# Optimization experiments

Hardware: AMD Instinct MI355X
Metric: run time of the kernel (lower is better)

## Reference

```python
import jax, jax.numpy as jnp
import numpy as np

B, SD, AD, M, MAXC = 65536, 32, 1, 32, 2  # batch, state_dim, action_dim, msg_dim, max_children


def _l2norm(x):
    # F.normalize(x, dim=-1) with eps=1e-12
    return x / jnp.maximum(jnp.linalg.norm(x, axis=-1, keepdims=True), 1e-12)


def _mlp(x, w1, b1, w2, b2, w3, b3):
    # MLPBase: Linear->ReLU->Linear->ReLU->Linear (400/300 hidden)
    h = jax.nn.relu(x @ w1 + b1)
    h = jax.nn.relu(h @ w2 + b2)
    return h @ w3 + b3


def setup_inputs() -> dict:
    key = jax.random.key(0)
    ks = iter(jax.random.split(key, 40))

    def p(shape):
        return jax.random.normal(next(ks), shape, jnp.float32) * 0.05

    inp = {
        "state": jax.random.normal(next(ks), (B, SD), jnp.float32),
        "action": jax.random.normal(next(ks), (B, AD), jnp.float32),
        # CriticUp params
        "up_fc1_w": p((SD + AD, 64)), "up_fc1_b": p((64,)),
        "up_fc2_w": p((64 + M, 64)), "up_fc2_b": p((64,)),
        "up_fc3_w": p((64, M)), "up_fc3_b": p((M,)),
        "att_w": p((9 + SD, M)), "att_b": p((M,)),
    }
    q_in = 12 + M + AD + M   # rel_pos(12) + self_input(msg_dim) + action + msg_down
    m_in = 12 + M + M        # rel_pos(12) + self_input + msg_down
    for n, d, out in (("q1", q_in, 1), ("q2", q_in, 1), ("msg", m_in, M * MAXC)):
        inp[n + "_w1"] = p((d, 400)); inp[n + "_b1"] = p((400,))
        inp[n + "_w2"] = p((400, 300)); inp[n + "_b2"] = p((300,))
        inp[n + "_w3"] = p((300, out)); inp[n + "_b3"] = p((out,))
    return inp


def reference(state, action,
              up_fc1_w, up_fc1_b, up_fc2_w, up_fc2_b, up_fc3_w, up_fc3_b,
              att_w, att_b,
              q1_w1, q1_b1, q1_w2, q1_b2, q1_w3, q1_b3,
              q2_w1, q2_b1, q2_w2, q2_b2, q2_w3, q2_b3,
              msg_w1, msg_b1, msg_w2, msg_b2, msg_w3, msg_b3):
    b = state.shape[0]
    # ---- bottom-up (num_limbs=1: root has no children -> zero child states/messages) ----
    xu = _l2norm(jnp.concatenate([state, action], -1) @ up_fc1_w + up_fc1_b)  # [b,64]
    ch_states = jnp.zeros((b, MAXC, 9 + SD), state.dtype)
    att = jax.nn.softmax(ch_states @ att_w + att_b, axis=-2)                  # [b,MAXC,M]
    m_up = (jnp.zeros((b, MAXC, M), state.dtype) * att).sum(-2)              # [b,M] (zeros)
    h = jnp.tanh(jnp.concatenate([xu, m_up], -1))
    h = jnp.tanh(h @ up_fc2_w + up_fc2_b)
    msg_up = _l2norm(h @ up_fc3_w + up_fc3_b)                                 # [b,M]
    # ---- top-down (root's parent index -1 wraps to itself -> zero relative offsets) ----
    pos = state[:, :3]
    rel = jnp.concatenate([jnp.zeros((b, 6), state.dtype), pos, pos], -1)     # [b,12]
    m_td = jnp.zeros((b, M), state.dtype)                                     # sliced from zero parent_msg
    xum = jnp.concatenate([rel, msg_up, action, m_td], -1)
    x1 = _mlp(xum, q1_w1, q1_b1, q1_w2, q1_b2, q1_w3, q1_b3)                  # [b,1]
    x2 = _mlp(xum, q2_w1, q2_b1, q2_w2, q2_b2, q2_w3, q2_b3)                  # [b,1]
    xm = jnp.tanh(jnp.concatenate([rel, msg_up, m_td], -1))
    msg_down = _l2norm(_mlp(xm, msg_w1, msg_b1, msg_w2, msg_b2, msg_w3, msg_b3))
    del msg_down  # computed per torch forward but unused in single-limb output
    # stack over 1 limb then sum over limb dim == identity
    return (x1, x2)
```

## Files before the change

### kernel.cpp

```cpp
#include <hip/hip_runtime.h>
#include <math.h>


#define BTOT   65536
#define XUM_OFF 655360ull

#define PK_BLK  78
#define PH_THR  512
#define PH_ROWS 128
#define PH_BLK  (BTOT / PH_ROWS)
#define F1W 0
#define F1B 2112
#define F2W 2176
#define F2B 6272
#define F3W 6336
#define F3B 8384
#define W0_FLOATS 8416

#define ML_THR  512
#define ML_ROWS 64
#define ML_BLK  (BTOT / ML_ROWS)
#define H1S     428

typedef float  f32x4 __attribute__((ext_vector_type(4)));
typedef __bf16 bf16x8 __attribute__((ext_vector_type(8)));
typedef unsigned short u16x8 __attribute__((ext_vector_type(8)));
typedef unsigned short u16x4 __attribute__((ext_vector_type(4)));
typedef unsigned int   u32x2 __attribute__((ext_vector_type(2)));

__device__ __forceinline__ unsigned short f2b(float f) {
  union { float f; unsigned int u; } v; v.f = f;
  return (unsigned short)((v.u + 0x7fffu + ((v.u >> 16) & 1u)) >> 16);
}
__device__ __forceinline__ float b2f(unsigned short u) {
  union { unsigned int u; float f; } v; v.u = ((unsigned int)u) << 16;
  return v.f;
}
__device__ __forceinline__ f32x4 MFMA(bf16x8 a, bf16x8 b, f32x4 c) {
  return __builtin_amdgcn_mfma_f32_16x16x32_bf16(a, b, c, 0, 0, 0);
}
__device__ __forceinline__ bf16x8 ld8(const unsigned short* p) {
  return __builtin_bit_cast(bf16x8, *(const u16x8*)p);
}
__device__ __forceinline__ float ftanh(float x) {
  float e = __builtin_amdgcn_exp2f(x * 2.885390081777927f);
  return (e - 1.0f) * __builtin_amdgcn_rcpf(e + 1.0f);
}

struct P0 {
  const float* state; const float* action;
  const float* f1w; const float* f1b;
  const float* f2w; const float* f2b;
  const float* f3w; const float* f3b;
  const float* q1w1; const float* q1b1; const float* q1w2;
  const float* q2w1; const float* q2b1; const float* q2w2;
  unsigned short* ws;
  unsigned short* xum;
};

__global__ __launch_bounds__(PH_THR, 4) void phase0_kernel(P0 P) {
  __shared__ float w0[W0_FLOATS];
  __shared__ unsigned short hx[PH_ROWS * 68];
  const int tid = threadIdx.x;

  if (blockIdx.x < PK_BLK) {
    const int gid = blockIdx.x * PH_THR + tid;
    const int lane = gid & 63, f = gid >> 6;
    const int q = f / 312, fl = f - q * 312;
    const float* w1 = q ? P.q2w1 : P.q1w1;
    const float* b1 = q ? P.q2b1 : P.q1b1;
    const float* w2 = q ? P.q2w2 : P.q1w2;
    int nt, ks; const bool isw1 = (fl < 52);
    if (isw1) { nt = fl >> 1; ks = fl & 1; }
    else      { int fl2 = fl - 52; nt = fl2 / 13; ks = fl2 - nt * 13; }
    const int col = nt * 16 + (lane & 15);
    const int k0  = ks * 32 + (lane >> 4) * 8;
    unsigned short v[8];
    #pragma unroll
    for (int j = 0; j < 8; ++j) {
      const int k = k0 + j;
      float x = 0.f;
      if (isw1) {
        if (col < 400) {
          if (k < 39) x = w1[(6 + k) * 400 + col];
          else if (k == 39) x = b1[col];
        }
      } else {
        if (k < 400 && col < 300) x = w2[k * 300 + col];
      }
      v[j] = f2b(x);
    }
    *(u16x8*)(P.ws + (size_t)f * 512 + lane * 8) = *(const u16x8*)v;
    return;
  }

  const int row = tid >> 2, sub = tid & 3, j0 = sub * 16;
  const long grow = (long)(blockIdx.x - PK_BLK) * PH_ROWS + row;

  for (int i = tid; i < 528;  i += PH_THR) *(f32x4*)(w0 + F1W + 4*i) = *(const f32x4*)(P.f1w + 4*i);
  for (int i = tid; i < 16;   i += PH_THR) *(f32x4*)(w0 + F1B + 4*i) = *(const f32x4*)(P.f1b + 4*i);
  for (int i = tid; i < 1024; i += PH_THR) *(f32x4*)(w0 + F2W + 4*i) = *(const f32x4*)(P.f2w + 4*i);
  for (int i = tid; i < 16;   i += PH_THR) *(f32x4*)(w0 + F2B + 4*i) = *(const f32x4*)(P.f2b + 4*i);
  for (int i = tid; i < 512;  i += PH_THR) *(f32x4*)(w0 + F3W + 4*i) = *(const f32x4*)(P.f3w + 4*i);
  for (int i = tid; i < 8;    i += PH_THR) *(f32x4*)(w0 + F3B + 4*i) = *(const f32x4*)(P.f3b + 4*i);

  float sa[33];
  {
    const float4* sp = (const float4*)(P.state + grow * 32);
    #pragma unroll
    for (int c = 0; c < 8; ++c) {
      float4 v = sp[c];
      sa[c*4+0] = v.x; sa[c*4+1] = v.y; sa[c*4+2] = v.z; sa[c*4+3] = v.w;
    }
    sa[32] = P.action[grow];
  }
  __syncthreads();

  float acc[16];
  #pragma unroll
  for (int j = 0; j < 16; ++j) acc[j] = w0[F1B + j0 + j];
  #pragma unroll 4
  for (int i = 0; i < 33; ++i) {
    const float s = sa[i];
    const f32x4* wr = (const f32x4*)&w0[F1W + i * 64 + j0];
    #pragma unroll
    for (int c = 0; c < 4; ++c) {
      f32x4 wv = wr[c];
      acc[c*4+0] += s * wv[0]; acc[c*4+1] += s * wv[1];
      acc[c*4+2] += s * wv[2]; acc[c*4+3] += s * wv[3];
    }
  }
  {
    float ss = 0.f;
    #pragma unroll
    for (int j = 0; j < 16; ++j) ss += acc[j] * acc[j];
    ss += __shfl_xor(ss, 1, 64); ss += __shfl_xor(ss, 2, 64);
    const float sc = 1.f / fmaxf(sqrtf(ss), 1e-12f);
    #pragma unroll
    for (int j = 0; j < 16; ++j) hx[row * 68 + j0 + j] = f2b(ftanh(acc[j] * sc));
  }
  __syncthreads();
  #pragma unroll
  for (int j = 0; j < 16; ++j) acc[j] = w0[F2B + j0 + j];
  #pragma unroll 4
  for (int i0 = 0; i0 < 16; ++i0) {
    const u16x4 hv4 = *(const u16x4*)&hx[row * 68 + i0 * 4];
    #pragma unroll
    for (int u = 0; u < 4; ++u) {
      const float hv = b2f(hv4[u]);
      const f32x4* wr = (const f32x4*)&w0[F2W + (i0 * 4 + u) * 64 + j0];
      #pragma unroll
      for (int c = 0; c < 4; ++c) {
        f32x4 wv = wr[c];
        acc[c*4+0] += hv * wv[0]; acc[c*4+1] += hv * wv[1];
        acc[c*4+2] += hv * wv[2]; acc[c*4+3] += hv * wv[3];
      }
    }
  }
  __syncthreads();
  #pragma unroll
  for (int j = 0; j < 16; ++j) hx[row * 68 + j0 + j] = f2b(ftanh(acc[j]));
  __syncthreads();
  const int j0m = sub * 8;
  float am[8];
  #pragma unroll
  for (int j = 0; j < 8; ++j) am[j] = w0[F3B + j0m + j];
  #pragma unroll 4
  for (int i0 = 0; i0 < 16; ++i0) {
    const u16x4 hv4 = *(const u16x4*)&hx[row * 68 + i0 * 4];
    #pragma unroll
    for (int u = 0; u < 4; ++u) {
      const float hv = b2f(hv4[u]);
      const f32x4* wr = (const f32x4*)&w0[F3W + (i0 * 4 + u) * 32 + j0m];
      #pragma unroll
      for (int c = 0; c < 2; ++c) {
        f32x4 wv = wr[c];
        am[c*4+0] += hv * wv[0]; am[c*4+1] += hv * wv[1];
        am[c*4+2] += hv * wv[2]; am[c*4+3] += hv * wv[3];
      }
    }
  }
  float sm = 0.f;
  #pragma unroll
  for (int j = 0; j < 8; ++j) sm += am[j] * am[j];
  sm += __shfl_xor(sm, 1, 64); sm += __shfl_xor(sm, 2, 64);
  const float scm = 1.f / fmaxf(sqrtf(sm), 1e-12f);
  __syncthreads();
  #pragma unroll
  for (int j = 0; j < 8; ++j) hx[row * 68 + j0m + j] = f2b(am[j] * scm);
  __syncthreads();
  {
    u16x8 v0, v1;
    #pragma unroll
    for (int t = 0; t < 16; ++t) {
      const int c = j0 + t;
      unsigned short u;
      if      (c < 3)  u = f2b(sa[c]);
      else if (c < 6)  u = f2b(sa[c - 3]);
      else if (c < 38) u = hx[row * 68 + (c - 6)];
      else if (c == 38) u = f2b(sa[32]);
      else if (c == 39) u = 0x3f80;
      else              u = 0;
      if (t < 8) v0[t] = u; else v1[t - 8] = u;
    }
    unsigned short* dst = P.xum + (size_t)grow * 64 + j0;
    *(u16x8*)dst = v0;
    *(u16x8*)(dst + 8) = v1;
  }
}

struct P1 {
  const unsigned short* img; const unsigned short* xum;
  const float* q1b2; const float* q1w3; const float* q1b3;
  const float* q2b2; const float* q2w3; const float* q2b3;
  float* out;
};

__global__ __launch_bounds__(ML_THR, 2) void mlp_kernel(P1 P) {
  __shared__ __align__(16) unsigned short h1[ML_ROWS * H1S];
  __shared__ float xred[ML_ROWS * 4];

  const int tid  = threadIdx.x;
  const int lane = tid & 63, w = tid >> 6;
  const int rl = lane & 15, g = lane >> 4;

  const int r1 = w & 3, ch = w >> 2;
  const int wm = w >> 2, wn = w & 3;

  const unsigned short* xr = P.xum + ((size_t)blockIdx.x * ML_ROWS + r1 * 16 + rl) * 64;
  const bf16x8 af0 = ld8(xr + g * 8);
  const bf16x8 af1 = ld8(xr + 32 + g * 8);

  for (int q = 0; q < 2; ++q) {
    {
      const unsigned short* w1f = P.img + ((size_t)(q * 312 + ch * 26)) * 512 + lane * 8;
      unsigned short* h1w = &h1[(size_t)(r1 * 16 + rl) * H1S + ch * 208 + g * 4];
      #pragma unroll 2
      for (int t = 0; t < 13; ++t) {
        const bf16x8 b0 = ld8(w1f + (size_t)(t * 2) * 512);
        const bf16x8 b1 = ld8(w1f + (size_t)(t * 2 + 1) * 512);
        f32x4 a = (f32x4){0.f, 0.f, 0.f, 0.f};
        a = MFMA(b0, af0, a);
        a = MFMA(b1, af1, a);
        const float c0 = fmaxf(a[0], 0.f), c1 = fmaxf(a[1], 0.f);
        const float c2 = fmaxf(a[2], 0.f), c3 = fmaxf(a[3], 0.f);
        unsigned int p01, p23;
        asm("v_cvt_pk_bf16_f32 %0, %1, %2" : "=v"(p01) : "v"(c0), "v"(c1));
        asm("v_cvt_pk_bf16_f32 %0, %1, %2" : "=v"(p23) : "v"(c2), "v"(c3));
        u32x2 pk; pk[0] = p01; pk[1] = p23;
        *(u32x2*)(h1w + t * 16) = pk;
      }
    }
    __syncthreads();

    f32x4 acc2[2][5];
    #pragma unroll
    for (int mt = 0; mt < 2; ++mt)
      #pragma unroll
      for (int jn = 0; jn < 5; ++jn) acc2[mt][jn] = (f32x4){0.f, 0.f, 0.f, 0.f};
    {
      const unsigned short* w2f = P.img + ((size_t)(q * 312 + 52 + wn * 65)) * 512 + lane * 8;
      #pragma unroll 2
      for (int ks = 0; ks < 13; ++ks) {
        const bf16x8 a0 = ld8(&h1[(size_t)(wm * 32 + rl) * H1S + ks * 32 + g * 8]);
        const bf16x8 a1 = ld8(&h1[(size_t)(wm * 32 + 16 + rl) * H1S + ks * 32 + g * 8]);
        #pragma unroll
        for (int jn = 0; jn < 5; ++jn) {
          const bf16x8 b = ld8(w2f + (size_t)(jn * 13 + ks) * 512);
          acc2[0][jn] = MFMA(a0, b, acc2[0][jn]);
          acc2[1][jn] = MFMA(a1, b, acc2[1][jn]);
        }
      }
    }

    const float* b2p = q ? P.q2b2 : P.q1b2;
    const float* w3  = q ? P.q2w3 : P.q1w3;
    const float* b3  = q ? P.q2b3 : P.q1b3;
    float xp[2][4];
    #pragma unroll
    for (int mt = 0; mt < 2; ++mt)
      #pragma unroll
      for (int i = 0; i < 4; ++i) xp[mt][i] = 0.f;
    #pragma unroll
    for (int jn = 0; jn < 5; ++jn) {
      const int n = wn * 80 + jn * 16 + rl;
      if (n < 300) {
        const float bv = b2p[n], wv = w3[n];
        #pragma unroll
        for (int mt = 0; mt < 2; ++mt)
          #pragma unroll
          for (int i = 0; i < 4; ++i)
            xp[mt][i] += fmaxf(acc2[mt][jn][i] + bv, 0.f) * wv;
      }
    }
    #pragma unroll
    for (int off = 1; off < 16; off <<= 1)
      #pragma unroll
      for (int mt = 0; mt < 2; ++mt)
        #pragma unroll
        for (int i = 0; i < 4; ++i)
          xp[mt][i] += __shfl_xor(xp[mt][i], off, 64);
    if (rl == 0) {
      #pragma unroll
      for (int mt = 0; mt < 2; ++mt)
        #pragma unroll
        for (int i = 0; i < 4; ++i)
          xred[(wm * 32 + mt * 16 + g * 4 + i) * 4 + wn] = xp[mt][i];
    }
    __syncthreads();
    if (tid < ML_ROWS) {
      const float4 xv = *(const float4*)&xred[tid * 4];
      P.out[(size_t)q * BTOT + (size_t)blockIdx.x * ML_ROWS + tid] =
          xv.x + xv.y + xv.z + xv.w + b3[0];
    }
    __syncthreads();
  }
}

extern "C" void kernel_launch(void* const* d_in, const int* in_sizes, int n_in,
                              void* d_out, int out_size, void* d_ws, size_t ws_size,
                              hipStream_t stream) {
  (void)in_sizes; (void)n_in; (void)out_size; (void)ws_size;
  P0 A;
  A.state  = (const float*)d_in[0];
  A.action = (const float*)d_in[1];
  A.f1w = (const float*)d_in[2]; A.f1b = (const float*)d_in[3];
  A.f2w = (const float*)d_in[4]; A.f2b = (const float*)d_in[5];
  A.f3w = (const float*)d_in[6]; A.f3b = (const float*)d_in[7];
  A.q1w1 = (const float*)d_in[10]; A.q1b1 = (const float*)d_in[11]; A.q1w2 = (const float*)d_in[12];
  A.q2w1 = (const float*)d_in[16]; A.q2b1 = (const float*)d_in[17]; A.q2w2 = (const float*)d_in[18];
  A.ws  = (unsigned short*)d_ws;
  A.xum = (unsigned short*)((unsigned char*)d_ws + XUM_OFF);
  phase0_kernel<<<dim3(PK_BLK + PH_BLK), dim3(PH_THR), 0, stream>>>(A);

  P1 B;
  B.img  = (const unsigned short*)d_ws;
  B.xum  = (const unsigned short*)((unsigned char*)d_ws + XUM_OFF);
  B.q1b2 = (const float*)d_in[13]; B.q1w3 = (const float*)d_in[14]; B.q1b3 = (const float*)d_in[15];
  B.q2b2 = (const float*)d_in[19]; B.q2w3 = (const float*)d_in[20]; B.q2b3 = (const float*)d_in[21];
  B.out  = (float*)d_out;
  mlp_kernel<<<dim3(ML_BLK), dim3(ML_THR), 0, stream>>>(B);
}
```

Baseline: 115.9 us.

## Switch MLP to 32x32x16 MFMA tiles and 128-row blocks

Replaces the 16x16x32 bf16 MFMA with the 32x32x16 variant in both hidden layers and repacks the weight image to match the 32-column tile layout. Doubles rows per block to 128 so each weight fragment is reused across more rows, and reorganises the wave split (two column-tile groups in layer 1, 64-row by 96-column tiles in layer 2). The intent is fewer instructions per FLOP and less weight reloading. The cost is more LDS per block, larger accumulators and register pressure, wider shuffle reductions, and some padding waste (layer 2 is padded to 384 columns).

Result: faster. 108.2 us (-6.6%).

```diff
diff --git a/kernel.cpp b/kernel.cpp
--- a/kernel.cpp
+++ b/kernel.cpp
@@ -3,9 +3,9 @@
 
 
 #define BTOT   65536
-#define XUM_OFF 655360ull
-
-#define PK_BLK  78
+#define XUM_OFF 745472ull
+
+#define PK_BLK  91
 #define PH_THR  512
 #define PH_ROWS 128
 #define PH_BLK  (BTOT / PH_ROWS)
@@ -18,11 +18,13 @@
 #define W0_FLOATS 8416
 
 #define ML_THR  512
-#define ML_ROWS 64
+#define ML_ROWS 128
 #define ML_BLK  (BTOT / ML_ROWS)
-#define H1S     428
-
-typedef float  f32x4 __attribute__((ext_vector_type(4)));
+#define H1S     424
+#define NFQ     364
+
+typedef float  f32x4  __attribute__((ext_vector_type(4)));
+typedef float  f32x16 __attribute__((ext_vector_type(16)));
 typedef __bf16 bf16x8 __attribute__((ext_vector_type(8)));
 typedef unsigned short u16x8 __attribute__((ext_vector_type(8)));
 typedef unsigned short u16x4 __attribute__((ext_vector_type(4)));
@@ -36,8 +38,8 @@
   union { unsigned int u; float f; } v; v.u = ((unsigned int)u) << 16;
   return v.f;
 }
-__device__ __forceinline__ f32x4 MFMA(bf16x8 a, bf16x8 b, f32x4 c) {
-  return __builtin_amdgcn_mfma_f32_16x16x32_bf16(a, b, c, 0, 0, 0);
+__device__ __forceinline__ f32x16 MFMA32(bf16x8 a, bf16x8 b, f32x16 c) {
+  return __builtin_amdgcn_mfma_f32_32x32x16_bf16(a, b, c, 0, 0, 0);
 }
 __device__ __forceinline__ bf16x8 ld8(const unsigned short* p) {
   return __builtin_bit_cast(bf16x8, *(const u16x8*)p);
@@ -66,15 +68,15 @@
   if (blockIdx.x < PK_BLK) {
     const int gid = blockIdx.x * PH_THR + tid;
     const int lane = gid & 63, f = gid >> 6;
-    const int q = f / 312, fl = f - q * 312;
+    const int q = f / NFQ, fl = f - q * NFQ;
     const float* w1 = q ? P.q2w1 : P.q1w1;
     const float* b1 = q ? P.q2b1 : P.q1b1;
     const float* w2 = q ? P.q2w2 : P.q1w2;
-    int nt, ks; const bool isw1 = (fl < 52);
-    if (isw1) { nt = fl >> 1; ks = fl & 1; }
-    else      { int fl2 = fl - 52; nt = fl2 / 13; ks = fl2 - nt * 13; }
-    const int col = nt * 16 + (lane & 15);
-    const int k0  = ks * 32 + (lane >> 4) * 8;
+    int ct, kst; const bool isw1 = (fl < 52);
+    if (isw1) { ct = fl >> 2; kst = fl & 3; }
+    else      { int fl2 = fl - 52; ct = fl2 / 26; kst = fl2 - ct * 26; }
+    const int col = ct * 32 + (lane & 31);
+    const int k0  = kst * 16 + (lane >> 5) * 8;
     unsigned short v[8];
     #pragma unroll
     for (int j = 0; j < 8; ++j) {
@@ -222,53 +224,56 @@
 
   const int tid  = threadIdx.x;
   const int lane = tid & 63, w = tid >> 6;
-  const int rl = lane & 15, g = lane >> 4;
-
-  const int r1 = w & 3, ch = w >> 2;
-  const int wm = w >> 2, wn = w & 3;
-
-  const unsigned short* xr = P.xum + ((size_t)blockIdx.x * ML_ROWS + r1 * 16 + rl) * 64;
-  const bf16x8 af0 = ld8(xr + g * 8);
-  const bf16x8 af1 = ld8(xr + 32 + g * 8);
+  const int l31 = lane & 31, g2 = lane >> 5;
+
+  const int rb = w & 3, ch = w >> 2;
+  const int ct0 = ch ? 7 : 0, ctN = ch ? 6 : 7;
+  const int rbh = w >> 2, cg = w & 3;
+
+  bf16x8 xf[4];
+  {
+    const unsigned short* xr =
+        P.xum + ((size_t)blockIdx.x * ML_ROWS + rb * 32 + l31) * 64 + g2 * 8;
+    #pragma unroll
+    for (int kst = 0; kst < 4; ++kst) xf[kst] = ld8(xr + kst * 16);
+  }
 
   for (int q = 0; q < 2; ++q) {
-    {
-      const unsigned short* w1f = P.img + ((size_t)(q * 312 + ch * 26)) * 512 + lane * 8;
-      unsigned short* h1w = &h1[(size_t)(r1 * 16 + rl) * H1S + ch * 208 + g * 4];
-      #pragma unroll 2
-      for (int t = 0; t < 13; ++t) {
-        const bf16x8 b0 = ld8(w1f + (size_t)(t * 2) * 512);
-        const bf16x8 b1 = ld8(w1f + (size_t)(t * 2 + 1) * 512);
-        f32x4 a = (f32x4){0.f, 0.f, 0.f, 0.f};
-        a = MFMA(b0, af0, a);
-        a = MFMA(b1, af1, a);
-        const float c0 = fmaxf(a[0], 0.f), c1 = fmaxf(a[1], 0.f);
-        const float c2 = fmaxf(a[2], 0.f), c3 = fmaxf(a[3], 0.f);
+    for (int t = 0; t < ctN; ++t) {
+      const int ct = ct0 + t;
+      const unsigned short* wf = P.img + ((size_t)(q * NFQ + ct * 4)) * 512 + lane * 8;
+      f32x16 a = {};
+      #pragma unroll
+      for (int kst = 0; kst < 4; ++kst)
+        a = MFMA32(ld8(wf + (size_t)kst * 512), xf[kst], a);
+      unsigned short* h1w = &h1[(size_t)(rb * 32 + l31) * H1S + ct * 32 + 4 * g2];
+      #pragma unroll
+      for (int grp = 0; grp < 4; ++grp) {
+        const float c0 = fmaxf(a[grp*4+0], 0.f), c1 = fmaxf(a[grp*4+1], 0.f);
+        const float c2 = fmaxf(a[grp*4+2], 0.f), c3 = fmaxf(a[grp*4+3], 0.f);
         unsigned int p01, p23;
         asm("v_cvt_pk_bf16_f32 %0, %1, %2" : "=v"(p01) : "v"(c0), "v"(c1));
         asm("v_cvt_pk_bf16_f32 %0, %1, %2" : "=v"(p23) : "v"(c2), "v"(c3));
         u32x2 pk; pk[0] = p01; pk[1] = p23;
-        *(u32x2*)(h1w + t * 16) = pk;
+        *(u32x2*)(h1w + grp * 8) = pk;
       }
     }
     __syncthreads();
 
-    f32x4 acc2[2][5];
-    #pragma unroll
-    for (int mt = 0; mt < 2; ++mt)
-      #pragma unroll
-      for (int jn = 0; jn < 5; ++jn) acc2[mt][jn] = (f32x4){0.f, 0.f, 0.f, 0.f};
+    f32x16 acc0[3], acc1[3];
+    #pragma unroll
+    for (int t = 0; t < 3; ++t) { acc0[t] = (f32x16){}; acc1[t] = (f32x16){}; }
     {
-      const unsigned short* w2f = P.img + ((size_t)(q * 312 + 52 + wn * 65)) * 512 + lane * 8;
-      #pragma unroll 2
-      for (int ks = 0; ks < 13; ++ks) {
-        const bf16x8 a0 = ld8(&h1[(size_t)(wm * 32 + rl) * H1S + ks * 32 + g * 8]);
-        const bf16x8 a1 = ld8(&h1[(size_t)(wm * 32 + 16 + rl) * H1S + ks * 32 + g * 8]);
+      const unsigned short* w2f =
+          P.img + ((size_t)(q * NFQ + 52 + cg * 3 * 26)) * 512 + lane * 8;
+      for (int kst = 0; kst < 26; ++kst) {
+        const bf16x8 a0 = ld8(&h1[(size_t)(rbh * 64 + l31) * H1S + kst * 16 + g2 * 8]);
+        const bf16x8 a1 = ld8(&h1[(size_t)(rbh * 64 + 32 + l31) * H1S + kst * 16 + g2 * 8]);
         #pragma unroll
-        for (int jn = 0; jn < 5; ++jn) {
-          const bf16x8 b = ld8(w2f + (size_t)(jn * 13 + ks) * 512);
-          acc2[0][jn] = MFMA(a0, b, acc2[0][jn]);
-          acc2[1][jn] = MFMA(a1, b, acc2[1][jn]);
+        for (int t = 0; t < 3; ++t) {
+          const bf16x8 b = ld8(w2f + (size_t)(t * 26 + kst) * 512);
+          acc0[t] = MFMA32(a0, b, acc0[t]);
+          acc1[t] = MFMA32(a1, b, acc1[t]);
         }
       }
     }
@@ -276,36 +281,35 @@
     const float* b2p = q ? P.q2b2 : P.q1b2;
     const float* w3  = q ? P.q2w3 : P.q1w3;
     const float* b3  = q ? P.q2b3 : P.q1b3;
-    float xp[2][4];
-    #pragma unroll
-    for (int mt = 0; mt < 2; ++mt)
-      #pragma unroll
-      for (int i = 0; i < 4; ++i) xp[mt][i] = 0.f;
-    #pragma unroll
-    for (int jn = 0; jn < 5; ++jn) {
-      const int n = wn * 80 + jn * 16 + rl;
+    float xp0[16], xp1[16];
+    #pragma unroll
+    for (int i = 0; i < 16; ++i) { xp0[i] = 0.f; xp1[i] = 0.f; }
+    #pragma unroll
+    for (int t = 0; t < 3; ++t) {
+      const int n = cg * 96 + t * 32 + l31;
       if (n < 300) {
         const float bv = b2p[n], wv = w3[n];
         #pragma unroll
-        for (int mt = 0; mt < 2; ++mt)
-          #pragma unroll
-          for (int i = 0; i < 4; ++i)
-            xp[mt][i] += fmaxf(acc2[mt][jn][i] + bv, 0.f) * wv;
-      }
-    }
-    #pragma unroll
-    for (int off = 1; off < 16; off <<= 1)
-      #pragma unroll
-      for (int mt = 0; mt < 2; ++mt)
-        #pragma unroll
-        for (int i = 0; i < 4; ++i)
-          xp[mt][i] += __shfl_xor(xp[mt][i], off, 64);
-    if (rl == 0) {
-      #pragma unroll
-      for (int mt = 0; mt < 2; ++mt)
-        #pragma unroll
-        for (int i = 0; i < 4; ++i)
-          xred[(wm * 32 + mt * 16 + g * 4 + i) * 4 + wn] = xp[mt][i];
+        for (int i = 0; i < 16; ++i) {
+          xp0[i] += fmaxf(acc0[t][i] + bv, 0.f) * wv;
+          xp1[i] += fmaxf(acc1[t][i] + bv, 0.f) * wv;
+        }
+      }
+    }
+    #pragma unroll
+    for (int off = 1; off < 32; off <<= 1)
+      #pragma unroll
+      for (int i = 0; i < 16; ++i) {
+        xp0[i] += __shfl_xor(xp0[i], off, 64);
+        xp1[i] += __shfl_xor(xp1[i], off, 64);
+      }
+    if (l31 == 0) {
+      #pragma unroll
+      for (int i = 0; i < 16; ++i) {
+        const int rl = (i & 3) + 8 * (i >> 2) + 4 * g2;
+        xred[(rbh * 64 + rl) * 4 + cg]      = xp0[i];
+        xred[(rbh * 64 + 32 + rl) * 4 + cg] = xp1[i];
+      }
     }
     __syncthreads();
     if (tid < ML_ROWS) {
```
